# Kernel tuning notes

Measured on AMD Instinct MI355X. Metric: run time of the kernel, lower is better.

Reference implementation:

```python
import jax, jax.numpy as jnp
import numpy as np

N_E = 1024     # codebook size (n_e, nbooks=1)
E_DIM = 256    # embedding dim
BETA = 0.25
B, T = 16, 4096


def setup_inputs() -> dict:
    key = jax.random.key(0)
    k1, k2 = jax.random.split(key)
    z = jax.random.normal(k1, (B, T, E_DIM), dtype=jnp.float32)
    # matches torch init: uniform(-1/n_e_i, 1/n_e_i)
    codebook = jax.random.uniform(k2, (N_E, E_DIM), dtype=jnp.float32,
                                  minval=-1.0 / N_E, maxval=1.0 / N_E)
    return {"z": z, "codebook": codebook}


def reference(z, codebook):
    zf = z.reshape(-1, E_DIM)                                   # [N, d]
    dist = (jnp.sum(zf * zf, axis=1, keepdims=True)
            - 2.0 * (zf @ codebook.T)
            + jnp.sum(codebook * codebook, axis=1)[None, :])
    idx = jnp.argmin(dist, axis=1)                              # [N]
    # one-hot scatter + matmul == codebook gather
    z_q = codebook[idx].reshape(z.shape)                        # [B, T, d]
    loss = (jnp.mean((z_q - jax.lax.stop_gradient(z)) ** 2)
            + BETA * jnp.mean((z - jax.lax.stop_gradient(z_q)) ** 2))
    # straight-through estimator
    z_q_st = z + jax.lax.stop_gradient(z_q - z)
    indices = idx.reshape(z.shape[:-1] + (1,))                  # [B, T, 1]
    return z_q_st, loss, indices
```

## Files before the change

### kernel.cpp

```cpp
#include <hip/hip_runtime.h>
#include <hip/hip_bf16.h>
#include <math.h>

typedef __bf16 bf16x8 __attribute__((ext_vector_type(8)));
typedef float f32x4 __attribute__((ext_vector_type(4)));
typedef unsigned short u16x8 __attribute__((ext_vector_type(8)));

constexpr int EDIM = 256;
constexpr int NE = 1024;
constexpr int NROWS = 65536;
constexpr float BETA = 0.25f;

constexpr size_t A2T_OFF   = 0;
constexpr size_t A2T_SZ    = (size_t)512 * 16 * 8192;
constexpr size_t B2T_OFF   = A2T_OFF + A2T_SZ;
constexpr size_t B2T_SZ    = (size_t)8 * 16 * 8192;
constexpr size_t SZROW_OFF = B2T_OFF + B2T_SZ;
constexpr size_t SZABS_OFF = SZROW_OFF + 262144;
constexpr size_t CNORM_OFF = SZABS_OFF + 262144;
constexpr size_t BMAX_OFF  = CNORM_OFF + 4096;
constexpr size_t EMAX_OFF  = BMAX_OFF + 4096;
constexpr size_t CNT_OFF   = EMAX_OFF + 256;
constexpr size_t LIST_OFF  = CNT_OFF + 256;
constexpr size_t LPART_OFF = LIST_OFF + 262144;
constexpr size_t LP2_OFF   = LPART_OFF + 262144;
constexpr size_t WS_NEED   = LP2_OFF + 1024;

__device__ __forceinline__ unsigned short f32_to_bf16_rne(float f) {
    unsigned u = __float_as_uint(f);
    u += 0x7fffu + ((u >> 16) & 1u);
    return (unsigned short)(u >> 16);
}
__device__ __forceinline__ float bf16_to_f32(unsigned short h) {
    return __uint_as_float((unsigned)h << 16);
}

#define GLL16(g, l)                                                                   \
    __builtin_amdgcn_global_load_lds(                                                 \
        (const __attribute__((address_space(1))) unsigned int*)(g),                   \
        (__attribute__((address_space(3))) unsigned int*)(l), 16, 0, 0)

__global__ __launch_bounds__(256)
void p1_rowstats(const float* __restrict__ z, float* __restrict__ szrow,
                 float* __restrict__ szabs) {
    __shared__ float xr[4][256];
    __shared__ float rres[4][16];
    const int w = threadIdx.x >> 6, l = threadIdx.x & 63;
    const int row = blockIdx.x * 4 + w;
    const float4 v = reinterpret_cast<const float4*>(z + (size_t)row * EDIM)[l];
    *reinterpret_cast<float4*>(&xr[w][l * 4]) = v;
    float asum = fabsf(v.x) + fabsf(v.y) + fabsf(v.z) + fabsf(v.w);
    #pragma unroll
    for (int off = 32; off; off >>= 1) asum += __shfl_down(asum, off);
    __syncthreads();
    if (l < 16) {
        const float* x = xr[w] + (l >> 3) * 128;
        const int j = l & 7;
        float r = __fmul_rn(x[j], x[j]);
        for (int i = 8; i < 128; i += 8) r = __fadd_rn(r, __fmul_rn(x[i + j], x[i + j]));
        rres[w][l] = r;
    }
    __syncthreads();
    if (l == 0) {
        const float* rr = rres[w];
        float h0 = __fadd_rn(__fadd_rn(__fadd_rn(rr[0], rr[1]), __fadd_rn(rr[2], rr[3])),
                             __fadd_rn(__fadd_rn(rr[4], rr[5]), __fadd_rn(rr[6], rr[7])));
        float h1 = __fadd_rn(__fadd_rn(__fadd_rn(rr[8], rr[9]), __fadd_rn(rr[10], rr[11])),
                             __fadd_rn(__fadd_rn(rr[12], rr[13]), __fadd_rn(rr[14], rr[15])));
        szrow[row] = __fadd_rn(h0, h1);
        szabs[row] = asum;
    }
}

__global__ __launch_bounds__(64)
void p3_codebook(const float* __restrict__ cb, float* __restrict__ cnorm,
                 char* __restrict__ B2t, float* __restrict__ bmax) {
    __shared__ float xr[256];
    __shared__ float rres[16];
    __shared__ unsigned short ehi[256], elo[256];
    const int e = blockIdx.x, l = threadIdx.x;
    const float4 v = reinterpret_cast<const float4*>(cb + (size_t)e * EDIM)[l];
    *reinterpret_cast<float4*>(&xr[l * 4]) = v;
    float amax = fmaxf(fmaxf(fabsf(v.x), fabsf(v.y)), fmaxf(fabsf(v.z), fabsf(v.w)));
    #pragma unroll
    for (int off = 32; off; off >>= 1) amax = fmaxf(amax, __shfl_down(amax, off));
    __syncthreads();
    #pragma unroll
    for (int i = 0; i < 4; ++i) {
        const int idx = i * 64 + l;
        const float f = xr[idx];
        const unsigned short h = f32_to_bf16_rne(f);
        ehi[idx] = h;
        elo[idx] = f32_to_bf16_rne(f - bf16_to_f32(h));
    }
    if (l < 16) {
        const float* x = xr + (l >> 3) * 128;
        const int j = l & 7;
        float r = __fmul_rn(x[j], x[j]);
        for (int i = 8; i < 128; i += 8) r = __fadd_rn(r, __fmul_rn(x[i + j], x[i + j]));
        rres[l] = r;
    }
    __syncthreads();
    if (l == 0) {
        float h0 = __fadd_rn(__fadd_rn(__fadd_rn(rres[0], rres[1]), __fadd_rn(rres[2], rres[3])),
                             __fadd_rn(__fadd_rn(rres[4], rres[5]), __fadd_rn(rres[6], rres[7])));
        float h1 = __fadd_rn(__fadd_rn(__fadd_rn(rres[8], rres[9]), __fadd_rn(rres[10], rres[11])),
                             __fadd_rn(__fadd_rn(rres[12], rres[13]), __fadd_rn(rres[14], rres[15])));
        cnorm[e] = __fadd_rn(h0, h1);
        bmax[e] = amax;
    }
    {
        const int c = l >> 2, kgv = l & 3;
        const int colbase = ((c < 8) ? c * 32 : (c - 8) * 32) + kgv * 8;
        const unsigned short* src = (c < 8) ? ehi : elo;
        char* dst = B2t + ((((size_t)(e >> 7) * 16 + c) * 512 + (size_t)kgv * 128 + (e & 127)) * 16);
        *reinterpret_cast<uint4*>(dst) = *reinterpret_cast<const uint4*>(&src[colbase]);
    }
}

__global__ void k_emax(const float* __restrict__ bmax, float* __restrict__ emax, int* cnt) {
    __shared__ float red[256];
    if (threadIdx.x == 0) cnt[0] = 0;
    float m = 0.f;
    for (int i = threadIdx.x; i < NE; i += 256) m = fmaxf(m, bmax[i]);
    red[threadIdx.x] = m;
    __syncthreads();
    for (int h = 128; h; h >>= 1) {
        if (threadIdx.x < h) red[threadIdx.x] = fmaxf(red[threadIdx.x], red[threadIdx.x + h]);
        __syncthreads();
    }
    if (threadIdx.x == 0) emax[0] = red[0];
}

__global__ __launch_bounds__(256)
void p2_atile(const float* __restrict__ z, char* __restrict__ A2t) {
    __shared__ float t[128][66];
    const int mt = blockIdx.x, cq = blockIdx.y, tid = threadIdx.x;
    const int c0 = cq * 64;
    #pragma unroll
    for (int i = 0; i < 8; ++i) {
        const int fid = i * 256 + tid;
        const int r = fid >> 4, c4 = fid & 15;
        const float4 v = *reinterpret_cast<const float4*>(
            z + ((size_t)(mt * 128 + r)) * EDIM + c0 + c4 * 4);
        *reinterpret_cast<float4*>(&t[r][c4 * 4]) = v;
    }
    __syncthreads();
    #pragma unroll
    for (int i = 0; i < 8; ++i) {
        const int sid = i * 256 + tid;
        const int caq = sid >> 9, kgv = (sid >> 7) & 3, rw = sid & 127;
        const int coff = (caq & 1) * 32 + kgv * 8;
        const int ca = (caq < 2) ? (cq * 2 + caq) : (8 + cq * 2 + (caq - 2));
        u16x8 out;
        #pragma unroll
        for (int j = 0; j < 8; ++j) {
            const float f = t[rw][coff + j];
            unsigned short h = f32_to_bf16_rne(f);
            if (caq >= 2) h = f32_to_bf16_rne(f - bf16_to_f32(h));
            out[j] = h;
        }
        char* dst = A2t + ((((size_t)mt * 16 + ca) * 512 + (size_t)kgv * 128 + rw) * 16);
        *reinterpret_cast<u16x8*>(dst) = out;
    }
}

__global__ __launch_bounds__(256, 1)
void vq_main(const char* __restrict__ A2t, const char* __restrict__ B2t,
             const float* __restrict__ cnorm, const float* __restrict__ szrow,
             const float* __restrict__ szabs, const float* __restrict__ emaxp,
             const float* __restrict__ cb,
             float* __restrict__ idxf, int* __restrict__ cnt, int* __restrict__ list,
             float* __restrict__ zq, float* __restrict__ lpart) {
    constexpr int RING = 131072;
    constexpr int CNS  = 155648;
    __shared__ char smem[159744] __attribute__((aligned(16)));
    float* cns = reinterpret_cast<float*>(smem + CNS);
    float (*ms1)[2] = reinterpret_cast<float(*)[2]>(smem);
    float (*ms2)[2] = reinterpret_cast<float(*)[2]>(smem + 1024);
    int   (*mi1)[2] = reinterpret_cast<int(*)[2]>(smem + 2048);
    int*  bidx      = reinterpret_cast<int*>(smem + 3072);

    const int tid = threadIdx.x;
    const int mtile = blockIdx.x;
    const size_t rowbase = (size_t)mtile * 128;
    const int l = tid & 63, wid = tid >> 6;
    const int kg = l >> 4, li = l & 15;
    const int wr = wid >> 1, wc = wid & 1;

    GLL16((const char*)cnorm + tid * 16, smem + CNS + tid * 16);
    const char* Ag = A2t + (size_t)mtile * 131072;
    #pragma unroll
    for (int i = 0; i < 32; ++i)
        GLL16(Ag + (i * 256 + tid) * 16, smem + (i * 256 + tid) * 16);
    #pragma unroll
    for (int c = 0; c < 3; ++c) {
        const char* gb = B2t + (size_t)c * 8192;
        char* lb = smem + RING + c * 8192;
        GLL16(gb + tid * 16, lb + tid * 16);
        GLL16(gb + (tid + 256) * 16, lb + (tid + 256) * 16);
    }
    asm volatile("s_waitcnt vmcnt(0)" ::: "memory");
    __builtin_amdgcn_s_barrier();

    int aoff[4], boff[4];
    #pragma unroll
    for (int f = 0; f < 4; ++f) {
        aoff[f] = kg * 2048 + (wr * 64 + f * 16 + li) * 16;
        boff[f] = kg * 2048 + (wc * 64 + f * 16 + li) * 16;
    }

    bf16x8 cAh[4], cAl[4], cB[4];
    #pragma unroll
    for (int f = 0; f < 4; ++f) {
        cAh[f] = *reinterpret_cast<const bf16x8*>(smem + 0 * 8192 + aoff[f]);
        cAl[f] = *reinterpret_cast<const bf16x8*>(smem + 8 * 8192 + aoff[f]);
        cB[f]  = *reinterpret_cast<const bf16x8*>(smem + RING + 0 * 8192 + boff[f]);
    }

    float s1v[4][4], s2v[4][4];
    int i1v[4][4];
    #pragma unroll
    for (int a = 0; a < 4; ++a)
        #pragma unroll
        for (int b = 0; b < 4; ++b) { s1v[a][b] = 3.4e38f; s2v[a][b] = 3.4e38f; i1v[a][b] = 0; }

    for (int nt = 0; nt < 8; ++nt) {
        int ntm3 = nt; if (ntm3 >= 6) ntm3 -= 6; else if (ntm3 >= 3) ntm3 -= 3;
        f32x4 acc[4][4];
        const f32x4 zf4 = {0.f, 0.f, 0.f, 0.f};
        #pragma unroll
        for (int a = 0; a < 4; ++a)
            #pragma unroll
            for (int b = 0; b < 4; ++b) acc[a][b] = zf4;

        #pragma unroll
        for (int j = 0; j < 16; ++j) {
            if (nt == 7 && j >= 14) asm volatile("s_waitcnt vmcnt(0)" ::: "memory");
            else                    asm volatile("s_waitcnt vmcnt(2)" ::: "memory");
            asm volatile("s_waitcnt lgkmcnt(0)" ::: "memory");
            __builtin_amdgcn_s_barrier();
            if (!(nt == 7 && j >= 13)) {
                const int gs = nt * 16 + j + 3;
                int ss = ntm3 + (j % 3);
                if (ss >= 3) ss -= 3;
                const char* gb = B2t + (size_t)gs * 8192;
                char* lb = smem + RING + ss * 8192;
                GLL16(gb + tid * 16, lb + tid * 16);
                GLL16(gb + (tid + 256) * 16, lb + (tid + 256) * 16);
            }
            bf16x8 nAh[4], nAl[4], nB[4];
            if (!(nt == 7 && j == 15)) {
                const int jn = (j + 1) & 15;
                int sp = ntm3 + ((j + 1) % 3);
                if (sp >= 3) sp -= 3;
                const char* Bb = smem + RING + sp * 8192;
                #pragma unroll
                for (int f = 0; f < 4; ++f)
                    nB[f] = *reinterpret_cast<const bf16x8*>(Bb + boff[f]);
                if (jn < 8) {
                    #pragma unroll
                    for (int f = 0; f < 4; ++f) {
                        nAh[f] = *reinterpret_cast<const bf16x8*>(smem + jn * 8192 + aoff[f]);
                        nAl[f] = *reinterpret_cast<const bf16x8*>(smem + (8 + jn) * 8192 + aoff[f]);
                    }
                } else {
                    #pragma unroll
                    for (int f = 0; f < 4; ++f)
                        nAh[f] = *reinterpret_cast<const bf16x8*>(smem + (jn - 8) * 8192 + aoff[f]);
                }
            }
            #pragma unroll
            for (int fm = 0; fm < 4; ++fm)
                #pragma unroll
                for (int fn = 0; fn < 4; ++fn)
                    acc[fm][fn] = __builtin_amdgcn_mfma_f32_16x16x32_bf16(cAh[fm], cB[fn], acc[fm][fn], 0, 0, 0);
            if (j < 8) {
                #pragma unroll
                for (int fm = 0; fm < 4; ++fm)
                    #pragma unroll
                    for (int fn = 0; fn < 4; ++fn)
                        acc[fm][fn] = __builtin_amdgcn_mfma_f32_16x16x32_bf16(cAl[fm], cB[fn], acc[fm][fn], 0, 0, 0);
            }
            #pragma unroll
            for (int f = 0; f < 4; ++f) { cAh[f] = nAh[f]; cAl[f] = nAl[f]; cB[f] = nB[f]; }
        }

        const int ntb = nt * 128;
        #pragma unroll
        for (int fn = 0; fn < 4; ++fn) {
            const int e = ntb + wc * 64 + fn * 16 + li;
            const float cn = cns[e];
            #pragma unroll
            for (int fm = 0; fm < 4; ++fm)
                #pragma unroll
                for (int r = 0; r < 4; ++r) {
                    const float s = cn - 2.0f * acc[fm][fn][r];
                    if (s < s1v[fm][r]) { s2v[fm][r] = s1v[fm][r]; s1v[fm][r] = s; i1v[fm][r] = e; }
                    else s2v[fm][r] = fminf(s2v[fm][r], s);
                }
        }
    }

    __syncthreads();

    #pragma unroll
    for (int fm = 0; fm < 4; ++fm)
        #pragma unroll
        for (int r = 0; r < 4; ++r) {
            float s1 = s1v[fm][r], s2 = s2v[fm][r];
            int i1 = i1v[fm][r];
            #pragma unroll
            for (int off = 1; off < 16; off <<= 1) {
                const float os1 = __shfl_xor(s1, off);
                const float os2 = __shfl_xor(s2, off);
                const int oi1 = __shfl_xor(i1, off);
                const bool take = (os1 < s1) || (os1 == s1 && oi1 < i1);
                const float loser = take ? s1 : os1;
                if (take) { s1 = os1; i1 = oi1; }
                s2 = fminf(fminf(s2, os2), loser);
            }
            if (li == 0) {
                const int rloc = wr * 64 + fm * 16 + (kg << 2) + r;
                ms1[rloc][wc] = s1; ms2[rloc][wc] = s2; mi1[rloc][wc] = i1;
            }
        }
    __syncthreads();

    if (tid < 128) {
        const float a1 = ms1[tid][0], b1 = ms1[tid][1];
        const float a2 = ms2[tid][0], b2 = ms2[tid][1];
        const int ai = mi1[tid][0], bi = mi1[tid][1];
        const bool take = (b1 < a1) || (b1 == a1 && bi < ai);
        const float s1 = take ? b1 : a1;
        const int i1 = take ? bi : ai;
        const float loser = take ? a1 : b1;
        const float s2 = fminf(fminf(a2, b2), loser);
        const int rowg = (int)rowbase + tid;
        const float szv = szrow[rowg], sab = szabs[rowg];
        const float M = 2.0e-4f * sab * emaxp[0] + ldexpf(1.0f, ilogbf(szv * 1.02f) - 23);
        idxf[rowg] = (float)i1;
        lpart[rowg] = s1 + szv;
        bidx[tid] = i1;
        if (s2 - s1 <= 2.0f * M) { const int p = atomicAdd(cnt, 1); list[p] = rowg; }
    }
    __syncthreads();

    {
        const float4* cb4 = reinterpret_cast<const float4*>(cb);
        float4* zq4 = reinterpret_cast<float4*>(zq);
        #pragma unroll 4
        for (int j = 0; j < 32; ++j) {
            const int rr = wid * 32 + j;
            const int e = bidx[rr];
            zq4[(rowbase + rr) * 64 + l] = cb4[(size_t)e * 64 + l];
        }
    }
}

__global__ __launch_bounds__(256)
void vq_rescan(const float* __restrict__ z, const float* __restrict__ cb,
               const float* __restrict__ cnorm, const float* __restrict__ szrow,
               const int* __restrict__ list, const int* __restrict__ cntp,
               float* __restrict__ idxf, float* __restrict__ zq, float* __restrict__ lpart) {
    __shared__ float zr[8][260];
    __shared__ float szs[8];
    __shared__ int rows_s[8];
    __shared__ float sred[256];
    __shared__ int ired[256];
    const int tid = threadIdx.x;
    const int n = cntp[0];
    const int groups = (n + 7) >> 3;
    for (int g = blockIdx.x; g < groups; g += gridDim.x) {
        if (tid < 8) {
            const int gi = g * 8 + tid;
            const int row = (gi < n) ? list[gi] : -1;
            rows_s[tid] = row;
            szs[tid] = (row >= 0) ? szrow[row] : 0.f;
        }
        __syncthreads();
        #pragma unroll
        for (int i = 0; i < 8; ++i) {
            const int sid = i * 256 + tid;
            const int rr = sid >> 8, k = sid & 255;
            if (rows_s[rr] >= 0) zr[rr][k] = z[(size_t)rows_s[rr] * EDIM + k];
        }
        __syncthreads();
        float bs[8];
        int bi[8];
        #pragma unroll
        for (int rr = 0; rr < 8; ++rr) { bs[rr] = 3.4e38f; bi[rr] = 0; }
        for (int q = 0; q < 4; ++q) {
            const int e = tid + q * 256;
            const float4* crow = reinterpret_cast<const float4*>(cb + (size_t)e * EDIM);
            float d[8];
            #pragma unroll
            for (int rr = 0; rr < 8; ++rr) d[rr] = 0.f;
            for (int k4 = 0; k4 < 64; ++k4) {
                const float4 c4 = crow[k4];
                #pragma unroll
                for (int rr = 0; rr < 8; ++rr) {
                    d[rr] = fmaf(zr[rr][k4 * 4 + 0], c4.x, d[rr]);
                    d[rr] = fmaf(zr[rr][k4 * 4 + 1], c4.y, d[rr]);
                    d[rr] = fmaf(zr[rr][k4 * 4 + 2], c4.z, d[rr]);
                    d[rr] = fmaf(zr[rr][k4 * 4 + 3], c4.w, d[rr]);
                }
            }
            const float cn = cnorm[e];
            #pragma unroll
            for (int rr = 0; rr < 8; ++rr) {
                const float b1 = __fadd_rn(szs[rr], __fmul_rn(-2.0f, d[rr]));
                const float s = __fadd_rn(b1, cn);
                if (s < bs[rr]) { bs[rr] = s; bi[rr] = e; }
            }
        }
        #pragma unroll
        for (int rr = 0; rr < 8; ++rr) {
            sred[tid] = bs[rr];
            ired[tid] = bi[rr];
            __syncthreads();
            for (int h = 128; h; h >>= 1) {
                if (tid < h) {
                    const float so = sred[tid + h];
                    const int io = ired[tid + h];
                    if (so < sred[tid] || (so == sred[tid] && io < ired[tid])) {
                        sred[tid] = so; ired[tid] = io;
                    }
                }
                __syncthreads();
            }
            if (rows_s[rr] >= 0) {
                const int best = ired[0];
                const int row = rows_s[rr];
                zq[(size_t)row * EDIM + tid] = cb[(size_t)best * EDIM + tid];
                if (tid == 0) { idxf[row] = (float)best; lpart[row] = sred[0]; }
            }
            __syncthreads();
        }
    }
}

__global__ void vq_loss1(const float* __restrict__ lpart, float* __restrict__ lp2) {
    __shared__ float red[256];
    const int t = threadIdx.x;
    red[t] = lpart[blockIdx.x * 256 + t];
    __syncthreads();
    for (int h = 128; h; h >>= 1) {
        if (t < h) red[t] += red[t + h];
        __syncthreads();
    }
    if (t == 0) lp2[blockIdx.x] = red[0];
}
__global__ void vq_loss2(const float* __restrict__ lp2, float* __restrict__ outloss) {
    __shared__ float red[256];
    const int t = threadIdx.x;
    red[t] = lp2[t];
    __syncthreads();
    for (int h = 128; h; h >>= 1) {
        if (t < h) red[t] += red[t + h];
        __syncthreads();
    }
    if (t == 0) outloss[0] = red[0] * ((1.0f + BETA) / 16777216.0f);
}

__device__ __forceinline__ float np_sum128_sq(const float* __restrict__ x) {
    float r[8];
    #pragma unroll
    for (int j = 0; j < 8; ++j) r[j] = __fmul_rn(x[j], x[j]);
    #pragma unroll
    for (int i = 8; i < 128; i += 8)
        #pragma unroll
        for (int j = 0; j < 8; ++j) r[j] = __fadd_rn(r[j], __fmul_rn(x[i + j], x[i + j]));
    return __fadd_rn(__fadd_rn(__fadd_rn(r[0], r[1]), __fadd_rn(r[2], r[3])),
                     __fadd_rn(__fadd_rn(r[4], r[5]), __fadd_rn(r[6], r[7])));
}
__global__ void fb_prep(const float* __restrict__ z, const float* __restrict__ cb,
                        float* __restrict__ szrow, float* __restrict__ cnorm) {
    int t = blockIdx.x * blockDim.x + threadIdx.x;
    if (t < NROWS) {
        const float* x = z + (size_t)t * EDIM;
        szrow[t] = __fadd_rn(np_sum128_sq(x), np_sum128_sq(x + 128));
    } else if (t < NROWS + NE) {
        const float* x = cb + (size_t)(t - NROWS) * EDIM;
        cnorm[t - NROWS] = __fadd_rn(np_sum128_sq(x), np_sum128_sq(x + 128));
    }
}
__global__ __launch_bounds__(256, 2)
void fb_vq(const float* __restrict__ z, const float* __restrict__ cb,
           const float* __restrict__ cnorm, const float* __restrict__ szrow,
           float* __restrict__ zq, float* __restrict__ idxf, float* __restrict__ lpart) {
    __shared__ float As[64 * 268];
    __shared__ float Bs[32 * 68];
    __shared__ int bidx[64];
    __shared__ float lred[4];
    const int tid = threadIdx.x;
    const int tx = tid & 15, ty = tid >> 4;
    const size_t rowbase = (size_t)blockIdx.x * 64;
    const float4* zg = reinterpret_cast<const float4*>(z + rowbase * EDIM);
    #pragma unroll
    for (int it = 0; it < 16; ++it) {
        int id = it * 256 + tid;
        int r = id >> 6, c4 = id & 63;
        float4 v = zg[id];
        *reinterpret_cast<float4*>(&As[r * 268 + c4 * 4]) = v;
    }
    float sz[4];
    #pragma unroll
    for (int m = 0; m < 4; ++m) sz[m] = szrow[rowbase + ty * 4 + m];
    float bestS[4]; int bestI[4];
    #pragma unroll
    for (int m = 0; m < 4; ++m) { bestS[m] = 3.4e38f; bestI[m] = 0; }
    for (int nt = 0; nt < NE / 64; ++nt) {
        float acc[4][4];
        #pragma unroll
        for (int m = 0; m < 4; ++m)
            #pragma unroll
            for (int n = 0; n < 4; ++n) acc[m][n] = 0.f;
        const int ebase = nt * 64;
        for (int k0 = 0; k0 < EDIM; k0 += 32) {
            __syncthreads();
            #pragma unroll
            for (int i = 0; i < 8; ++i) {
                int id = i * 256 + tid;
                int n = id >> 5, k = id & 31;
                Bs[k * 68 + n] = cb[(size_t)(ebase + n) * EDIM + k0 + k];
            }
            __syncthreads();
            #pragma unroll
            for (int kg2 = 0; kg2 < 32; kg2 += 4) {
                float4 a[4], b[4];
                #pragma unroll
                for (int m = 0; m < 4; ++m)
                    a[m] = *reinterpret_cast<const float4*>(&As[(ty * 4 + m) * 268 + k0 + kg2]);
                #pragma unroll
                for (int kk = 0; kk < 4; ++kk)
                    b[kk] = *reinterpret_cast<const float4*>(&Bs[(kg2 + kk) * 68 + tx * 4]);
                #pragma unroll
                for (int m = 0; m < 4; ++m) {
                    const float* av = reinterpret_cast<const float*>(&a[m]);
                    #pragma unroll
                    for (int kk = 0; kk < 4; ++kk) {
                        acc[m][0] = fmaf(av[kk], b[kk].x, acc[m][0]);
                        acc[m][1] = fmaf(av[kk], b[kk].y, acc[m][1]);
                        acc[m][2] = fmaf(av[kk], b[kk].z, acc[m][2]);
                        acc[m][3] = fmaf(av[kk], b[kk].w, acc[m][3]);
                    }
                }
            }
        }
        #pragma unroll
        for (int n = 0; n < 4; ++n) {
            int e = ebase + tx * 4 + n;
            float cn = cnorm[e];
            #pragma unroll
            for (int m = 0; m < 4; ++m) {
                float b1 = __fadd_rn(sz[m], __fmul_rn(-2.0f, acc[m][n]));
                float s = __fadd_rn(b1, cn);
                if (s < bestS[m]) { bestS[m] = s; bestI[m] = e; }
            }
        }
    }
    #pragma unroll
    for (int m = 0; m < 4; ++m) {
        float s = bestS[m]; int i = bestI[m];
        #pragma unroll
        for (int off = 1; off < 16; off <<= 1) {
            float s2 = __shfl_xor(s, off);
            int i2 = __shfl_xor(i, off);
            if (s2 < s || (s2 == s && i2 < i)) { s = s2; i = i2; }
        }
        if (tx == 0) bidx[ty * 4 + m] = i;
    }
    __syncthreads();
    if (tid < 64) idxf[rowbase + tid] = (float)bidx[tid];
    float lsum = 0.f;
    for (int r = 0; r < 64; ++r) {
        int e = bidx[r];
        float c = cb[(size_t)e * EDIM + tid];
        float zv = As[r * 268 + tid];
        float d = c - zv;
        lsum = fmaf(d, d, lsum);
        zq[(rowbase + r) * EDIM + tid] = c;
    }
    #pragma unroll
    for (int off = 32; off; off >>= 1) lsum += __shfl_down(lsum, off);
    if ((tid & 63) == 0) lred[tid >> 6] = lsum;
    __syncthreads();
    if (tid == 0) lpart[blockIdx.x] = lred[0] + lred[1] + lred[2] + lred[3];
}
__global__ void fb_loss(const float* __restrict__ lpart, float* __restrict__ out_loss) {
    __shared__ float red[256];
    int tid = threadIdx.x;
    float s = 0.f;
    for (int i = tid; i < NROWS / 64; i += 256) s += lpart[i];
    red[tid] = s;
    __syncthreads();
    for (int h = 128; h; h >>= 1) {
        if (tid < h) red[tid] += red[tid + h];
        __syncthreads();
    }
    if (tid == 0) out_loss[0] = red[0] * (1.0f + BETA) / (float)((size_t)NROWS * EDIM);
}

extern "C" void kernel_launch(void* const* d_in, const int* in_sizes, int n_in,
                              void* d_out, int out_size, void* d_ws, size_t ws_size,
                              hipStream_t stream) {
    const float* z = (const float*)d_in[0];
    const float* cb = (const float*)d_in[1];
    float* out = (float*)d_out;
    float* zq = out;
    float* loss = out + (size_t)NROWS * EDIM;
    float* idxf = loss + 1;
    char* ws = (char*)d_ws;

    if (ws_size < WS_NEED) {
        float* cnorm = (float*)ws;
        float* szrow = cnorm + NE;
        float* lpart = szrow + NROWS;
        hipLaunchKernelGGL(fb_prep, dim3((NROWS + NE + 255) / 256), dim3(256), 0, stream, z, cb, szrow, cnorm);
        hipLaunchKernelGGL(fb_vq, dim3(NROWS / 64), dim3(256), 0, stream, z, cb, cnorm, szrow, zq, idxf, lpart);
        hipLaunchKernelGGL(fb_loss, dim3(1), dim3(256), 0, stream, lpart, loss);
        return;
    }

    char* A2t = ws + A2T_OFF;
    char* B2t = ws + B2T_OFF;
    float* szrow = (float*)(ws + SZROW_OFF);
    float* szabs = (float*)(ws + SZABS_OFF);
    float* cnorm = (float*)(ws + CNORM_OFF);
    float* bmax = (float*)(ws + BMAX_OFF);
    float* emax = (float*)(ws + EMAX_OFF);
    int* cnt = (int*)(ws + CNT_OFF);
    int* list = (int*)(ws + LIST_OFF);
    float* lpart = (float*)(ws + LPART_OFF);
    float* lp2 = (float*)(ws + LP2_OFF);

    hipLaunchKernelGGL(p1_rowstats, dim3(NROWS / 4), dim3(256), 0, stream, z, szrow, szabs);
    hipLaunchKernelGGL(p3_codebook, dim3(NE), dim3(64), 0, stream, cb, cnorm, B2t, bmax);
    hipLaunchKernelGGL(k_emax, dim3(1), dim3(256), 0, stream, bmax, emax, cnt);
    hipLaunchKernelGGL(p2_atile, dim3(512, 4), dim3(256), 0, stream, z, A2t);
    hipLaunchKernelGGL(vq_main, dim3(512), dim3(256), 0, stream,
                       A2t, B2t, cnorm, szrow, szabs, emax, cb, idxf, cnt, list, zq, lpart);
    hipLaunchKernelGGL(vq_rescan, dim3(1024), dim3(256), 0, stream,
                       z, cb, cnorm, szrow, list, cnt, idxf, zq, lpart);
    hipLaunchKernelGGL(vq_loss1, dim3(256), dim3(256), 0, stream, lpart, lp2);
    hipLaunchKernelGGL(vq_loss2, dim3(1), dim3(256), 0, stream, lp2, loss);
}
```

Baseline: 257.8 us.

## Fuse row statistics into A-tile prep and stream codebook tiles from global

The separate row-statistics kernel is removed. Its squared-norm and abs-sum computation now runs inside p2_atile, which processes full 64-row stripes, so z is read once instead of twice. In vq_main, the three-slot LDS ring buffer for codebook tiles is dropped, along with its per-step waitcnt and barrier. B fragments are instead loaded directly from global memory (likely L2-resident) one step ahead, which cuts synchronisation and LDS use but exposes global-load latency inside the MFMA loop.

Result: faster. 243.0 us (-5.8%).

```diff
diff --git a/kernel.cpp b/kernel.cpp
--- a/kernel.cpp
+++ b/kernel.cpp
@@ -40,38 +40,6 @@
         (const __attribute__((address_space(1))) unsigned int*)(g),                   \
         (__attribute__((address_space(3))) unsigned int*)(l), 16, 0, 0)
 
-__global__ __launch_bounds__(256)
-void p1_rowstats(const float* __restrict__ z, float* __restrict__ szrow,
-                 float* __restrict__ szabs) {
-    __shared__ float xr[4][256];
-    __shared__ float rres[4][16];
-    const int w = threadIdx.x >> 6, l = threadIdx.x & 63;
-    const int row = blockIdx.x * 4 + w;
-    const float4 v = reinterpret_cast<const float4*>(z + (size_t)row * EDIM)[l];
-    *reinterpret_cast<float4*>(&xr[w][l * 4]) = v;
-    float asum = fabsf(v.x) + fabsf(v.y) + fabsf(v.z) + fabsf(v.w);
-    #pragma unroll
-    for (int off = 32; off; off >>= 1) asum += __shfl_down(asum, off);
-    __syncthreads();
-    if (l < 16) {
-        const float* x = xr[w] + (l >> 3) * 128;
-        const int j = l & 7;
-        float r = __fmul_rn(x[j], x[j]);
-        for (int i = 8; i < 128; i += 8) r = __fadd_rn(r, __fmul_rn(x[i + j], x[i + j]));
-        rres[w][l] = r;
-    }
-    __syncthreads();
-    if (l == 0) {
-        const float* rr = rres[w];
-        float h0 = __fadd_rn(__fadd_rn(__fadd_rn(rr[0], rr[1]), __fadd_rn(rr[2], rr[3])),
-                             __fadd_rn(__fadd_rn(rr[4], rr[5]), __fadd_rn(rr[6], rr[7])));
-        float h1 = __fadd_rn(__fadd_rn(__fadd_rn(rr[8], rr[9]), __fadd_rn(rr[10], rr[11])),
-                             __fadd_rn(__fadd_rn(rr[12], rr[13]), __fadd_rn(rr[14], rr[15])));
-        szrow[row] = __fadd_rn(h0, h1);
-        szabs[row] = asum;
-    }
-}
-
 __global__ __launch_bounds__(64)
 void p3_codebook(const float* __restrict__ cb, float* __restrict__ cnorm,
                  char* __restrict__ B2t, float* __restrict__ bmax) {
@@ -133,34 +101,61 @@
 }
 
 __global__ __launch_bounds__(256)
-void p2_atile(const float* __restrict__ z, char* __restrict__ A2t) {
-    __shared__ float t[128][66];
-    const int mt = blockIdx.x, cq = blockIdx.y, tid = threadIdx.x;
-    const int c0 = cq * 64;
-    #pragma unroll
-    for (int i = 0; i < 8; ++i) {
+void p2_atile(const float* __restrict__ z, char* __restrict__ A2t,
+              float* __restrict__ szrow, float* __restrict__ szabs) {
+    __shared__ float t[64][260];
+    __shared__ float ch[64][16];
+    const int mt = blockIdx.x, h = blockIdx.y, tid = threadIdx.x;
+    const int row0 = mt * 128 + h * 64;
+    #pragma unroll
+    for (int i = 0; i < 16; ++i) {
         const int fid = i * 256 + tid;
-        const int r = fid >> 4, c4 = fid & 15;
+        const int r = fid >> 6, c4 = fid & 63;
         const float4 v = *reinterpret_cast<const float4*>(
-            z + ((size_t)(mt * 128 + r)) * EDIM + c0 + c4 * 4);
+            z + (size_t)(row0 + r) * EDIM + c4 * 4);
         *reinterpret_cast<float4*>(&t[r][c4 * 4]) = v;
     }
     __syncthreads();
-    #pragma unroll
-    for (int i = 0; i < 8; ++i) {
+    {
+        const int r = tid >> 2, q = tid & 3;
+        float asum = 0.f;
+        for (int c = 0; c < 64; ++c) asum += fabsf(t[r][q * 64 + c]);
+        asum += __shfl_xor(asum, 1);
+        asum += __shfl_xor(asum, 2);
+        #pragma unroll
+        for (int cc = 0; cc < 4; ++cc) {
+            const int chain = q * 4 + cc;
+            const float* x = &t[r][(chain >> 3) * 128];
+            const int j = chain & 7;
+            float rr = __fmul_rn(x[j], x[j]);
+            for (int i = 8; i < 128; i += 8) rr = __fadd_rn(rr, __fmul_rn(x[i + j], x[i + j]));
+            ch[r][chain] = rr;
+        }
+        __syncthreads();
+        if (q == 0) {
+            const float* c0 = ch[r];
+            const float h0 = __fadd_rn(__fadd_rn(__fadd_rn(c0[0], c0[1]), __fadd_rn(c0[2], c0[3])),
+                                       __fadd_rn(__fadd_rn(c0[4], c0[5]), __fadd_rn(c0[6], c0[7])));
+            const float h1 = __fadd_rn(__fadd_rn(__fadd_rn(c0[8], c0[9]), __fadd_rn(c0[10], c0[11])),
+                                       __fadd_rn(__fadd_rn(c0[12], c0[13]), __fadd_rn(c0[14], c0[15])));
+            szrow[row0 + r] = __fadd_rn(h0, h1);
+            szabs[row0 + r] = asum;
+        }
+    }
+    #pragma unroll
+    for (int i = 0; i < 16; ++i) {
         const int sid = i * 256 + tid;
-        const int caq = sid >> 9, kgv = (sid >> 7) & 3, rw = sid & 127;
-        const int coff = (caq & 1) * 32 + kgv * 8;
-        const int ca = (caq < 2) ? (cq * 2 + caq) : (8 + cq * 2 + (caq - 2));
+        const int ca = sid >> 8, kgv = (sid >> 6) & 3, rwl = sid & 63;
+        const int cbase = ((ca < 8) ? ca : ca - 8) * 32 + kgv * 8;
         u16x8 out;
         #pragma unroll
         for (int j = 0; j < 8; ++j) {
-            const float f = t[rw][coff + j];
-            unsigned short h = f32_to_bf16_rne(f);
-            if (caq >= 2) h = f32_to_bf16_rne(f - bf16_to_f32(h));
-            out[j] = h;
-        }
-        char* dst = A2t + ((((size_t)mt * 16 + ca) * 512 + (size_t)kgv * 128 + rw) * 16);
+            const float f = t[rwl][cbase + j];
+            unsigned short h16 = f32_to_bf16_rne(f);
+            if (ca >= 8) h16 = f32_to_bf16_rne(f - bf16_to_f32(h16));
+            out[j] = h16;
+        }
+        char* dst = A2t + ((((size_t)mt * 16 + ca) * 512 + (size_t)kgv * 128 + (h * 64 + rwl)) * 16);
         *reinterpret_cast<u16x8*>(dst) = out;
     }
 }
@@ -172,9 +167,8 @@
              const float* __restrict__ cb,
              float* __restrict__ idxf, int* __restrict__ cnt, int* __restrict__ list,
              float* __restrict__ zq, float* __restrict__ lpart) {
-    constexpr int RING = 131072;
-    constexpr int CNS  = 155648;
-    __shared__ char smem[159744] __attribute__((aligned(16)));
+    constexpr int CNS = 131072;
+    __shared__ char smem[135168] __attribute__((aligned(16)));
     float* cns = reinterpret_cast<float*>(smem + CNS);
     float (*ms1)[2] = reinterpret_cast<float(*)[2]>(smem);
     float (*ms2)[2] = reinterpret_cast<float(*)[2]>(smem + 1024);
@@ -193,15 +187,8 @@
     #pragma unroll
     for (int i = 0; i < 32; ++i)
         GLL16(Ag + (i * 256 + tid) * 16, smem + (i * 256 + tid) * 16);
-    #pragma unroll
-    for (int c = 0; c < 3; ++c) {
-        const char* gb = B2t + (size_t)c * 8192;
-        char* lb = smem + RING + c * 8192;
-        GLL16(gb + tid * 16, lb + tid * 16);
-        GLL16(gb + (tid + 256) * 16, lb + (tid + 256) * 16);
-    }
     asm volatile("s_waitcnt vmcnt(0)" ::: "memory");
-    __builtin_amdgcn_s_barrier();
+    __syncthreads();
 
     int aoff[4], boff[4];
     #pragma unroll
@@ -215,7 +202,7 @@
     for (int f = 0; f < 4; ++f) {
         cAh[f] = *reinterpret_cast<const bf16x8*>(smem + 0 * 8192 + aoff[f]);
         cAl[f] = *reinterpret_cast<const bf16x8*>(smem + 8 * 8192 + aoff[f]);
-        cB[f]  = *reinterpret_cast<const bf16x8*>(smem + RING + 0 * 8192 + boff[f]);
+        cB[f]  = *reinterpret_cast<const bf16x8*>(B2t + boff[f]);
     }
 
     float s1v[4][4], s2v[4][4];
@@ -226,7 +213,6 @@
         for (int b = 0; b < 4; ++b) { s1v[a][b] = 3.4e38f; s2v[a][b] = 3.4e38f; i1v[a][b] = 0; }
 
     for (int nt = 0; nt < 8; ++nt) {
-        int ntm3 = nt; if (ntm3 >= 6) ntm3 -= 6; else if (ntm3 >= 3) ntm3 -= 3;
         f32x4 acc[4][4];
         const f32x4 zf4 = {0.f, 0.f, 0.f, 0.f};
         #pragma unroll
@@ -236,28 +222,14 @@
 
         #pragma unroll
         for (int j = 0; j < 16; ++j) {
-            if (nt == 7 && j >= 14) asm volatile("s_waitcnt vmcnt(0)" ::: "memory");
-            else                    asm volatile("s_waitcnt vmcnt(2)" ::: "memory");
-            asm volatile("s_waitcnt lgkmcnt(0)" ::: "memory");
-            __builtin_amdgcn_s_barrier();
-            if (!(nt == 7 && j >= 13)) {
-                const int gs = nt * 16 + j + 3;
-                int ss = ntm3 + (j % 3);
-                if (ss >= 3) ss -= 3;
-                const char* gb = B2t + (size_t)gs * 8192;
-                char* lb = smem + RING + ss * 8192;
-                GLL16(gb + tid * 16, lb + tid * 16);
-                GLL16(gb + (tid + 256) * 16, lb + (tid + 256) * 16);
-            }
+            const int g = nt * 16 + j;
             bf16x8 nAh[4], nAl[4], nB[4];
-            if (!(nt == 7 && j == 15)) {
+            {
                 const int jn = (j + 1) & 15;
-                int sp = ntm3 + ((j + 1) % 3);
-                if (sp >= 3) sp -= 3;
-                const char* Bb = smem + RING + sp * 8192;
+                const char* gB = B2t + (size_t)(g + 1) * 8192;
                 #pragma unroll
                 for (int f = 0; f < 4; ++f)
-                    nB[f] = *reinterpret_cast<const bf16x8*>(Bb + boff[f]);
+                    nB[f] = *reinterpret_cast<const bf16x8*>(gB + boff[f]);
                 if (jn < 8) {
                     #pragma unroll
                     for (int f = 0; f < 4; ++f) {
@@ -266,8 +238,10 @@
                     }
                 } else {
                     #pragma unroll
-                    for (int f = 0; f < 4; ++f)
+                    for (int f = 0; f < 4; ++f) {
                         nAh[f] = *reinterpret_cast<const bf16x8*>(smem + (jn - 8) * 8192 + aoff[f]);
+                        nAl[f] = cAl[f];
+                    }
                 }
             }
             #pragma unroll
@@ -635,10 +609,9 @@
     float* lpart = (float*)(ws + LPART_OFF);
     float* lp2 = (float*)(ws + LP2_OFF);
 
-    hipLaunchKernelGGL(p1_rowstats, dim3(NROWS / 4), dim3(256), 0, stream, z, szrow, szabs);
     hipLaunchKernelGGL(p3_codebook, dim3(NE), dim3(64), 0, stream, cb, cnorm, B2t, bmax);
     hipLaunchKernelGGL(k_emax, dim3(1), dim3(256), 0, stream, bmax, emax, cnt);
-    hipLaunchKernelGGL(p2_atile, dim3(512, 4), dim3(256), 0, stream, z, A2t);
+    hipLaunchKernelGGL(p2_atile, dim3(512, 2), dim3(256), 0, stream, z, A2t, szrow, szabs);
     hipLaunchKernelGGL(vq_main, dim3(512), dim3(256), 0, stream,
                        A2t, B2t, cnorm, szrow, szabs, emax, cb, idxf, cnt, list, zq, lpart);
     hipLaunchKernelGGL(vq_rescan, dim3(1024), dim3(256), 0, stream,
```
